# Performance work log

Measured on AMD Instinct MI355X. Metric: run time of the kernel, lower is better.

The kernel has to match this reference:

```python
import jax, jax.numpy as jnp
import numpy as np

NUM_SPECIES = 7
B, A, F = 1024, 48, 384


def setup_inputs() -> dict:
    key = jax.random.key(0)
    ks = jax.random.split(key, 10)
    species = jax.random.randint(ks[0], (B, A), 0, NUM_SPECIES, dtype=jnp.int32)
    aev = jax.random.normal(ks[1], (B, A, F), dtype=jnp.float32)
    def w(k, shape, fan_in):
        s = 1.0 / np.sqrt(fan_in).astype(np.float32)
        return jax.random.uniform(k, shape, jnp.float32, -s, s)
    return {
        "species": species,
        "aev": aev,
        "W1": w(ks[2], (NUM_SPECIES, 256, 384), 384),
        "b1": w(ks[3], (NUM_SPECIES, 256), 384),
        "W2": w(ks[4], (NUM_SPECIES, 192, 256), 256),
        "b2": w(ks[5], (NUM_SPECIES, 192), 256),
        "W3": w(ks[6], (NUM_SPECIES, 160, 192), 192),
        "b3": w(ks[7], (NUM_SPECIES, 160), 192),
        "W4": w(ks[8], (NUM_SPECIES, 1, 160), 160),
        "b4": w(ks[9], (NUM_SPECIES, 1), 160),
    }


def reference(species, aev, W1, b1, W2, b2, W3, b3, W4, b4):
    # species: [B, A] int, aev: [B, A, 384]
    celu = lambda x: jax.nn.celu(x, alpha=0.1)

    def expert(s):
        # Per-species MLP 384->256->192->160->1 applied to all atoms; selected via mask.
        h = celu(jnp.einsum('baf,hf->bah', aev, W1[s]) + b1[s])
        h = celu(jnp.einsum('bah,gh->bag', h, W2[s]) + b2[s])
        h = celu(jnp.einsum('bag,eg->bae', h, W3[s]) + b3[s])
        return (jnp.einsum('bae,oe->bao', h, W4[s]) + b4[s])[..., 0]  # [B, A]

    atom_energy = jnp.zeros(species.shape, aev.dtype)
    for s in range(NUM_SPECIES):  # fixed small expert loop (hard routing)
        atom_energy = jnp.where(species == s, expert(s), atom_energy)
    # scatter-sum atomic energies into per-molecule energies
    return atom_energy.sum(axis=1)  # [B]
```

## Files before the change

kernel.cpp:

```cpp
#include <hip/hip_runtime.h>
#include <math.h>

#define NSPEC 7
#define NMOL 1024
#define APM 48
#define NATOMS (NMOL * APM)
#define FDIM 384

typedef unsigned short u16;
typedef unsigned int u32;
typedef __attribute__((ext_vector_type(8))) short short8;
typedef __attribute__((ext_vector_type(4))) float floatx4;

#define W1_ELEMS_PER_S (16 * 12 * 64 * 8)
#define W2_ELEMS_PER_S (12 * 8 * 64 * 8)
#define W3_ELEMS_PER_S (10 * 6 * 64 * 8)

#define BUCKET_BLOCKS (NATOMS / 256)
#define PACK1_BLOCKS (NSPEC * 16)
#define PACK2_BLOCKS (NSPEC * 12)
#define PACK3_BLOCKS (NSPEC * 10)
#define PREP_BLOCKS (BUCKET_BLOCKS + PACK1_BLOCKS + PACK2_BLOCKS + PACK3_BLOCKS)

#define WS_W1_OFF 32
#define WS_W2_OFF (WS_W1_OFF + 1376256)
#define WS_W3_OFF (WS_W2_OFF + 688128)
#define WS_BKT_OFF (WS_W3_OFF + 430080)

#define BUFST 264

__device__ __forceinline__ float celu01(float x) {
    float e = fmaf(0.1f, __expf(x * 10.0f), -0.1f);
    return x > 0.0f ? x : e;
}

__device__ __forceinline__ u16 bfr(float f) {
    u32 u = __float_as_uint(f);
    u += 0x7fffu + ((u >> 16) & 1u);
    return (u16)(u >> 16);
}

__device__ __forceinline__ float bf2f(short s) {
    return __uint_as_float(((u32)(u16)s) << 16);
}

union U8 { short8 v; u16 u[8]; };

template <int KGS, int NTILES>
__device__ __forceinline__ void pack_tile(const float* __restrict__ W,
                                          u16* __restrict__ dst,
                                          int s, int t2, u16* lds) {
    const int K = KGS * 32;
    const int K4 = K / 4;
    int t = threadIdx.x;
    const float* wbase = W + ((size_t)(s * NTILES + t2) * 16) * K;
    for (int i = t; i < 16 * K4; i += 256) {
        int r = i / K4, c = i % K4;
        float4 v = ((const float4*)(wbase + (size_t)r * K))[c];
        u16* d = lds + r * K + c * 4;
        d[0] = bfr(v.x); d[1] = bfr(v.y); d[2] = bfr(v.z); d[3] = bfr(v.w);
    }
    __syncthreads();
    int w = t >> 6, lane = t & 63;
    int n = lane & 15, ks = lane >> 4;
    for (int kg = w; kg < KGS; kg += 4) {
        short8 v = *reinterpret_cast<const short8*>(lds + n * K + kg * 32 + ks * 8);
        *reinterpret_cast<short8*>(
            dst + (((size_t)(s * NTILES + t2) * KGS + kg) * 64 + lane) * 8) = v;
    }
}

__global__ void prep_kernel(const int* __restrict__ species,
                            int* __restrict__ g_cnt, u16* __restrict__ bucket,
                            const float* __restrict__ W1, const float* __restrict__ W2,
                            const float* __restrict__ W3,
                            u16* __restrict__ w1p, u16* __restrict__ w2p,
                            u16* __restrict__ w3p, float* __restrict__ out) {
    __shared__ u16 lds[16 * 384];
    __shared__ int l_cnt[NSPEC];
    __shared__ int l_base[NSPEC];
    int t = threadIdx.x;
    int bx = blockIdx.x;
    if (bx < BUCKET_BLOCKS) {
        if (bx == 0) {
            float4 z = {0.f, 0.f, 0.f, 0.f};
            ((float4*)out)[t] = z;
        }
        if (t < NSPEC) l_cnt[t] = 0;
        __syncthreads();
        int i = bx * 256 + t;
        int s = species[i];
        int lpos = atomicAdd(&l_cnt[s], 1);
        __syncthreads();
        if (t < NSPEC) l_base[t] = atomicAdd(&g_cnt[t], l_cnt[t]);
        __syncthreads();
        bucket[s * NATOMS + l_base[s] + lpos] = (u16)i;
    } else if (bx < BUCKET_BLOCKS + PACK1_BLOCKS) {
        int pid = bx - BUCKET_BLOCKS;
        pack_tile<12, 16>(W1, w1p, pid / 16, pid % 16, lds);
    } else if (bx < BUCKET_BLOCKS + PACK1_BLOCKS + PACK2_BLOCKS) {
        int pid = bx - (BUCKET_BLOCKS + PACK1_BLOCKS);
        pack_tile<8, 12>(W2, w2p, pid / 12, pid % 12, lds);
    } else {
        int pid = bx - (BUCKET_BLOCKS + PACK1_BLOCKS + PACK2_BLOCKS);
        pack_tile<6, 10>(W3, w3p, pid / 10, pid % 10, lds);
    }
}

template <int KGS, int NT, int NBUF>
__device__ __forceinline__ void run_layer(const short8* af0, const short8* af1,
                                          const u16* __restrict__ wsp,
                                          const float* __restrict__ bias,
                                          u16* __restrict__ outbuf, int lane) {
    const int nl = lane & 15, kg4 = lane >> 4;
    const u16* wb = wsp + (size_t)lane * 8;
    short8 b[NBUF][KGS];
#pragma unroll
    for (int p = 0; p < NBUF - 1; ++p)
#pragma unroll
        for (int kg = 0; kg < KGS; ++kg)
            b[p][kg] = *reinterpret_cast<const short8*>(wb + ((size_t)p * KGS + kg) * 512);
#pragma unroll
    for (int t = 0; t < NT; ++t) {
        int pre = t + NBUF - 1;
        if (pre < NT) {
            int slot = pre % NBUF;
#pragma unroll
            for (int kg = 0; kg < KGS; ++kg)
                b[slot][kg] = *reinterpret_cast<const short8*>(wb + ((size_t)pre * KGS + kg) * 512);
        }
        int cur = t % NBUF;
        floatx4 acc0 = {0.f, 0.f, 0.f, 0.f};
        floatx4 acc1 = {0.f, 0.f, 0.f, 0.f};
#pragma unroll
        for (int kg = 0; kg < KGS; ++kg) {
            acc0 = __builtin_amdgcn_mfma_f32_16x16x32_bf16(af0[kg], b[cur][kg], acc0, 0, 0, 0);
            acc1 = __builtin_amdgcn_mfma_f32_16x16x32_bf16(af1[kg], b[cur][kg], acc1, 0, 0, 0);
        }
        float bn = bias[t * 16 + nl];
#pragma unroll
        for (int r = 0; r < 4; ++r) {
            outbuf[(kg4 * 4 + r) * BUFST + t * 16 + nl] = bfr(celu01(acc0[r] + bn));
            outbuf[(16 + kg4 * 4 + r) * BUFST + t * 16 + nl] = bfr(celu01(acc1[r] + bn));
        }
    }
}

template <int KGS>
__device__ __forceinline__ void load_a_lds(const u16* __restrict__ buf,
                                           short8* af0, short8* af1, int lane) {
    int nl = lane & 15, kg4 = lane >> 4;
#pragma unroll
    for (int kg = 0; kg < KGS; ++kg) {
        af0[kg] = *reinterpret_cast<const short8*>(buf + (size_t)nl * BUFST + kg * 32 + kg4 * 8);
        af1[kg] = *reinterpret_cast<const short8*>(buf + (size_t)(16 + nl) * BUFST + kg * 32 + kg4 * 8);
    }
}

__global__ __launch_bounds__(128, 2) void mlp_kernel(
    const float* __restrict__ aev,
    const u16* __restrict__ w1p, const u16* __restrict__ w2p, const u16* __restrict__ w3p,
    const float* __restrict__ b1, const float* __restrict__ b2, const float* __restrict__ b3,
    const float* __restrict__ W4, const float* __restrict__ b4,
    const int* __restrict__ g_cnt, const u16* __restrict__ bucket,
    float* __restrict__ out) {
    int bx = blockIdx.x;
    int s = bx & 7;
    if (s >= NSPEC) return;
    int chunk = bx >> 3;
    int cnt = g_cnt[s];
    int w = threadIdx.x >> 6, lane = threadIdx.x & 63;
    int base = chunk * 64 + w * 32;
    if (base >= cnt) return;

    __shared__ __align__(16) u16 bufs[2][32 * BUFST];
    u16* buf = &bufs[w][0];

    int nl = lane & 15, kg4 = lane >> 4;

    short8 af0[12], af1[12];
    {
        int i0 = base + nl;       if (i0 >= cnt) i0 = cnt - 1;
        int i1 = base + 16 + nl;  if (i1 >= cnt) i1 = cnt - 1;
        int a0 = (int)bucket[s * NATOMS + i0];
        int a1 = (int)bucket[s * NATOMS + i1];
        const float* ar0 = aev + (size_t)a0 * FDIM;
        const float* ar1 = aev + (size_t)a1 * FDIM;
#pragma unroll
        for (int kg = 0; kg < 12; ++kg) {
            const float4* p0 = (const float4*)(ar0 + kg * 32 + kg4 * 8);
            const float4* p1 = (const float4*)(ar1 + kg * 32 + kg4 * 8);
            float4 a = p0[0], b = p0[1];
            float4 c = p1[0], d = p1[1];
            U8 x, y;
            x.u[0] = bfr(a.x); x.u[1] = bfr(a.y); x.u[2] = bfr(a.z); x.u[3] = bfr(a.w);
            x.u[4] = bfr(b.x); x.u[5] = bfr(b.y); x.u[6] = bfr(b.z); x.u[7] = bfr(b.w);
            y.u[0] = bfr(c.x); y.u[1] = bfr(c.y); y.u[2] = bfr(c.z); y.u[3] = bfr(c.w);
            y.u[4] = bfr(d.x); y.u[5] = bfr(d.y); y.u[6] = bfr(d.z); y.u[7] = bfr(d.w);
            af0[kg] = x.v;
            af1[kg] = y.v;
        }
    }
    run_layer<12, 16, 2>(af0, af1, w1p + (size_t)s * W1_ELEMS_PER_S, b1 + s * 256, buf, lane);

    short8 c0[8], c1[8];
    load_a_lds<8>(buf, c0, c1, lane);
    run_layer<8, 12, 3>(c0, c1, w2p + (size_t)s * W2_ELEMS_PER_S, b2 + s * 192, buf, lane);

    short8 d0[6], d1[6];
    load_a_lds<6>(buf, d0, d1, lane);
    run_layer<6, 10, 3>(d0, d1, w3p + (size_t)s * W3_ELEMS_PER_S, b3 + s * 160, buf, lane);

    {
        int m = lane >> 1, q = lane & 1;
        const u16* h = buf + (size_t)m * BUFST + q * 80;
        const float* w4s = W4 + s * 160 + q * 80;
        float p = 0.f;
#pragma unroll
        for (int c = 0; c < 10; ++c) {
            short8 hv = *reinterpret_cast<const short8*>(h + c * 8);
            const float4* wp4 = (const float4*)(w4s + c * 8);
            float4 wa = wp4[0], wb = wp4[1];
            p += bf2f(hv[0]) * wa.x + bf2f(hv[1]) * wa.y + bf2f(hv[2]) * wa.z + bf2f(hv[3]) * wa.w;
            p += bf2f(hv[4]) * wb.x + bf2f(hv[5]) * wb.y + bf2f(hv[6]) * wb.z + bf2f(hv[7]) * wb.w;
        }
        p += __shfl_down(p, 1, 2);
        int idx = base + m;
        if (q == 0 && idx < cnt) {
            int atom = (int)bucket[s * NATOMS + idx];
            atomicAdd(&out[atom / APM], p + b4[s]);
        }
    }
}

extern "C" void kernel_launch(void* const* d_in, const int* in_sizes, int n_in,
                              void* d_out, int out_size, void* d_ws, size_t ws_size,
                              hipStream_t stream) {
    const int* species = (const int*)d_in[0];
    const float* aev = (const float*)d_in[1];
    const float* W1 = (const float*)d_in[2];
    const float* b1 = (const float*)d_in[3];
    const float* W2 = (const float*)d_in[4];
    const float* b2 = (const float*)d_in[5];
    const float* W3 = (const float*)d_in[6];
    const float* b3 = (const float*)d_in[7];
    const float* W4 = (const float*)d_in[8];
    const float* b4 = (const float*)d_in[9];
    float* out = (float*)d_out;

    unsigned char* wsb = (unsigned char*)d_ws;
    int* g_cnt = (int*)wsb;
    u16* w1p = (u16*)(wsb + WS_W1_OFF);
    u16* w2p = (u16*)(wsb + WS_W2_OFF);
    u16* w3p = (u16*)(wsb + WS_W3_OFF);
    u16* bucket = (u16*)(wsb + WS_BKT_OFF);

    hipMemsetAsync(g_cnt, 0, 8 * sizeof(int), stream);

    prep_kernel<<<PREP_BLOCKS, 256, 0, stream>>>(
        species, g_cnt, bucket, W1, W2, W3, w1p, w2p, w3p, out);

    mlp_kernel<<<8 * (NATOMS / 64), 128, 0, stream>>>(
        aev, w1p, w2p, w3p, b1, b2, b3, W4, b4, g_cnt, bucket, out);
}
```

Before: 163.5 us.

## Fuse prep and MLP kernels into one cooperative persistent kernel with grid sync

Merges the bucketing/weight-packing kernel and the per-species MLP kernel into a single cooperative launch of 512 blocks of 128 threads, separated by a grid-wide sync. After the sync each block loops over up to 8 chunks of atoms for its species instead of launching one block per chunk. This removes a kernel launch and its inter-kernel gap, but it caps concurrency at 512 blocks, adds the cost of a grid barrier, and leaves fewer blocks doing the packing work.

```diff
diff --git a/kernel.cpp b/kernel.cpp
--- a/kernel.cpp
+++ b/kernel.cpp
@@ -1,5 +1,8 @@
 #include <hip/hip_runtime.h>
+#include <hip/hip_cooperative_groups.h>
 #include <math.h>
+
+namespace cg = cooperative_groups;
 
 #define NSPEC 7
 #define NMOL 1024
@@ -16,18 +19,15 @@
 #define W2_ELEMS_PER_S (12 * 8 * 64 * 8)
 #define W3_ELEMS_PER_S (10 * 6 * 64 * 8)
 
-#define BUCKET_BLOCKS (NATOMS / 256)
-#define PACK1_BLOCKS (NSPEC * 16)
-#define PACK2_BLOCKS (NSPEC * 12)
-#define PACK3_BLOCKS (NSPEC * 10)
-#define PREP_BLOCKS (BUCKET_BLOCKS + PACK1_BLOCKS + PACK2_BLOCKS + PACK3_BLOCKS)
-
 #define WS_W1_OFF 32
 #define WS_W2_OFF (WS_W1_OFF + 1376256)
 #define WS_W3_OFF (WS_W2_OFF + 688128)
 #define WS_BKT_OFF (WS_W3_OFF + 430080)
 
 #define BUFST 264
+#define GRID 512
+#define BUCKET_BLOCKS 384
+#define NTILE_TOTAL 266
 
 __device__ __forceinline__ float celu01(float x) {
     float e = fmaf(0.1f, __expf(x * 10.0f), -0.1f);
@@ -53,9 +53,9 @@
     const int K = KGS * 32;
     const int K4 = K / 4;
     int t = threadIdx.x;
-    const float* wbase = W + ((size_t)(s * NTILES + t2) * 16) * K;
-    for (int i = t; i < 16 * K4; i += 256) {
-        int r = i / K4, c = i % K4;
+    const float* wbase = W + (size_t)(s * NTILES + t2) * 16 * K;
+    for (int i = t; i < 16 * K4; i += 128) {
+        int r = i / K4, c = i - r * K4;
         float4 v = ((const float4*)(wbase + (size_t)r * K))[c];
         u16* d = lds + r * K + c * 4;
         d[0] = bfr(v.x); d[1] = bfr(v.y); d[2] = bfr(v.z); d[3] = bfr(v.w);
@@ -63,172 +63,173 @@
     __syncthreads();
     int w = t >> 6, lane = t & 63;
     int n = lane & 15, ks = lane >> 4;
-    for (int kg = w; kg < KGS; kg += 4) {
+    for (int kg = w; kg < KGS; kg += 2) {
         short8 v = *reinterpret_cast<const short8*>(lds + n * K + kg * 32 + ks * 8);
         *reinterpret_cast<short8*>(
             dst + (((size_t)(s * NTILES + t2) * KGS + kg) * 64 + lane) * 8) = v;
     }
-}
-
-__global__ void prep_kernel(const int* __restrict__ species,
-                            int* __restrict__ g_cnt, u16* __restrict__ bucket,
-                            const float* __restrict__ W1, const float* __restrict__ W2,
-                            const float* __restrict__ W3,
-                            u16* __restrict__ w1p, u16* __restrict__ w2p,
-                            u16* __restrict__ w3p, float* __restrict__ out) {
-    __shared__ u16 lds[16 * 384];
+    __syncthreads();
+}
+
+template <int KGS, int NT, int NBUF>
+__device__ __forceinline__ void run_layer(const short8* af0, const short8* af1,
+                                          const u16* wsp, const float* bias,
+                                          u16* outbuf, int lane) {
+    const int nl = lane & 15, kg4 = lane >> 4;
+    const u16* wb = wsp + (size_t)lane * 8;
+    short8 b[NBUF][KGS];
+#pragma unroll
+    for (int p = 0; p < NBUF - 1; ++p)
+#pragma unroll
+        for (int kg = 0; kg < KGS; ++kg)
+            b[p][kg] = *reinterpret_cast<const short8*>(wb + ((size_t)p * KGS + kg) * 512);
+#pragma unroll
+    for (int t = 0; t < NT; ++t) {
+        int pre = t + NBUF - 1;
+        if (pre < NT) {
+            int slot = pre % NBUF;
+#pragma unroll
+            for (int kg = 0; kg < KGS; ++kg)
+                b[slot][kg] = *reinterpret_cast<const short8*>(wb + ((size_t)pre * KGS + kg) * 512);
+        }
+        int cur = t % NBUF;
+        floatx4 acc0 = {0.f, 0.f, 0.f, 0.f};
+        floatx4 acc1 = {0.f, 0.f, 0.f, 0.f};
+#pragma unroll
+        for (int kg = 0; kg < KGS; ++kg) {
+            acc0 = __builtin_amdgcn_mfma_f32_16x16x32_bf16(af0[kg], b[cur][kg], acc0, 0, 0, 0);
+            acc1 = __builtin_amdgcn_mfma_f32_16x16x32_bf16(af1[kg], b[cur][kg], acc1, 0, 0, 0);
+        }
+        float bn = bias[t * 16 + nl];
+#pragma unroll
+        for (int r = 0; r < 4; ++r) {
+            outbuf[(kg4 * 4 + r) * BUFST + t * 16 + nl] = bfr(celu01(acc0[r] + bn));
+            outbuf[(16 + kg4 * 4 + r) * BUFST + t * 16 + nl] = bfr(celu01(acc1[r] + bn));
+        }
+    }
+}
+
+template <int KGS>
+__device__ __forceinline__ void load_a_lds(const u16* buf, short8* af0, short8* af1, int lane) {
+    int nl = lane & 15, kg4 = lane >> 4;
+#pragma unroll
+    for (int kg = 0; kg < KGS; ++kg) {
+        af0[kg] = *reinterpret_cast<const short8*>(buf + (size_t)nl * BUFST + kg * 32 + kg4 * 8);
+        af1[kg] = *reinterpret_cast<const short8*>(buf + (size_t)(16 + nl) * BUFST + kg * 32 + kg4 * 8);
+    }
+}
+
+__global__ __launch_bounds__(128, 2) void fused_kernel(
+    const int* species, const float* aev,
+    const float* W1, const float* W2, const float* W3,
+    const float* b1, const float* b2, const float* b3,
+    const float* W4, const float* b4,
+    int* g_cnt, u16* bucket,
+    u16* w1p, u16* w2p, u16* w3p,
+    float* out) {
+    __shared__ __align__(16) u16 smem[2 * 32 * BUFST];
     __shared__ int l_cnt[NSPEC];
     __shared__ int l_base[NSPEC];
+
+    int bx = blockIdx.x;
     int t = threadIdx.x;
-    int bx = blockIdx.x;
+
     if (bx < BUCKET_BLOCKS) {
         if (bx == 0) {
             float4 z = {0.f, 0.f, 0.f, 0.f};
             ((float4*)out)[t] = z;
+            ((float4*)out)[t + 128] = z;
         }
         if (t < NSPEC) l_cnt[t] = 0;
         __syncthreads();
-        int i = bx * 256 + t;
+        int i = bx * 128 + t;
         int s = species[i];
         int lpos = atomicAdd(&l_cnt[s], 1);
         __syncthreads();
         if (t < NSPEC) l_base[t] = atomicAdd(&g_cnt[t], l_cnt[t]);
         __syncthreads();
         bucket[s * NATOMS + l_base[s] + lpos] = (u16)i;
-    } else if (bx < BUCKET_BLOCKS + PACK1_BLOCKS) {
-        int pid = bx - BUCKET_BLOCKS;
-        pack_tile<12, 16>(W1, w1p, pid / 16, pid % 16, lds);
-    } else if (bx < BUCKET_BLOCKS + PACK1_BLOCKS + PACK2_BLOCKS) {
-        int pid = bx - (BUCKET_BLOCKS + PACK1_BLOCKS);
-        pack_tile<8, 12>(W2, w2p, pid / 12, pid % 12, lds);
     } else {
-        int pid = bx - (BUCKET_BLOCKS + PACK1_BLOCKS + PACK2_BLOCKS);
-        pack_tile<6, 10>(W3, w3p, pid / 10, pid % 10, lds);
-    }
-}
-
-template <int KGS, int NT, int NBUF>
-__device__ __forceinline__ void run_layer(const short8* af0, const short8* af1,
-                                          const u16* __restrict__ wsp,
-                                          const float* __restrict__ bias,
-                                          u16* __restrict__ outbuf, int lane) {
-    const int nl = lane & 15, kg4 = lane >> 4;
-    const u16* wb = wsp + (size_t)lane * 8;
-    short8 b[NBUF][KGS];
-#pragma unroll
-    for (int p = 0; p < NBUF - 1; ++p)
-#pragma unroll
-        for (int kg = 0; kg < KGS; ++kg)
-            b[p][kg] = *reinterpret_cast<const short8*>(wb + ((size_t)p * KGS + kg) * 512);
-#pragma unroll
-    for (int t = 0; t < NT; ++t) {
-        int pre = t + NBUF - 1;
-        if (pre < NT) {
-            int slot = pre % NBUF;
-#pragma unroll
-            for (int kg = 0; kg < KGS; ++kg)
-                b[slot][kg] = *reinterpret_cast<const short8*>(wb + ((size_t)pre * KGS + kg) * 512);
-        }
-        int cur = t % NBUF;
-        floatx4 acc0 = {0.f, 0.f, 0.f, 0.f};
-        floatx4 acc1 = {0.f, 0.f, 0.f, 0.f};
-#pragma unroll
-        for (int kg = 0; kg < KGS; ++kg) {
-            acc0 = __builtin_amdgcn_mfma_f32_16x16x32_bf16(af0[kg], b[cur][kg], acc0, 0, 0, 0);
-            acc1 = __builtin_amdgcn_mfma_f32_16x16x32_bf16(af1[kg], b[cur][kg], acc1, 0, 0, 0);
-        }
-        float bn = bias[t * 16 + nl];
-#pragma unroll
-        for (int r = 0; r < 4; ++r) {
-            outbuf[(kg4 * 4 + r) * BUFST + t * 16 + nl] = bfr(celu01(acc0[r] + bn));
-            outbuf[(16 + kg4 * 4 + r) * BUFST + t * 16 + nl] = bfr(celu01(acc1[r] + bn));
-        }
-    }
-}
-
-template <int KGS>
-__device__ __forceinline__ void load_a_lds(const u16* __restrict__ buf,
-                                           short8* af0, short8* af1, int lane) {
-    int nl = lane & 15, kg4 = lane >> 4;
-#pragma unroll
-    for (int kg = 0; kg < KGS; ++kg) {
-        af0[kg] = *reinterpret_cast<const short8*>(buf + (size_t)nl * BUFST + kg * 32 + kg4 * 8);
-        af1[kg] = *reinterpret_cast<const short8*>(buf + (size_t)(16 + nl) * BUFST + kg * 32 + kg4 * 8);
-    }
-}
-
-__global__ __launch_bounds__(128, 2) void mlp_kernel(
-    const float* __restrict__ aev,
-    const u16* __restrict__ w1p, const u16* __restrict__ w2p, const u16* __restrict__ w3p,
-    const float* __restrict__ b1, const float* __restrict__ b2, const float* __restrict__ b3,
-    const float* __restrict__ W4, const float* __restrict__ b4,
-    const int* __restrict__ g_cnt, const u16* __restrict__ bucket,
-    float* __restrict__ out) {
-    int bx = blockIdx.x;
+        for (int tile = bx - BUCKET_BLOCKS; tile < NTILE_TOTAL; tile += GRID - BUCKET_BLOCKS) {
+            if (tile < 112) {
+                pack_tile<12, 16>(W1, w1p, tile / 16, tile % 16, smem);
+            } else if (tile < 196) {
+                int u = tile - 112;
+                pack_tile<8, 12>(W2, w2p, u / 12, u % 12, smem);
+            } else {
+                int u = tile - 196;
+                pack_tile<6, 10>(W3, w3p, u / 10, u % 10, smem);
+            }
+        }
+    }
+
+    __threadfence();
+    cg::this_grid().sync();
+
     int s = bx & 7;
     if (s >= NSPEC) return;
-    int chunk = bx >> 3;
     int cnt = g_cnt[s];
-    int w = threadIdx.x >> 6, lane = threadIdx.x & 63;
-    int base = chunk * 64 + w * 32;
-    if (base >= cnt) return;
-
-    __shared__ __align__(16) u16 bufs[2][32 * BUFST];
-    u16* buf = &bufs[w][0];
-
+    int w = t >> 6, lane = t & 63;
     int nl = lane & 15, kg4 = lane >> 4;
-
-    short8 af0[12], af1[12];
-    {
-        int i0 = base + nl;       if (i0 >= cnt) i0 = cnt - 1;
-        int i1 = base + 16 + nl;  if (i1 >= cnt) i1 = cnt - 1;
-        int a0 = (int)bucket[s * NATOMS + i0];
-        int a1 = (int)bucket[s * NATOMS + i1];
-        const float* ar0 = aev + (size_t)a0 * FDIM;
-        const float* ar1 = aev + (size_t)a1 * FDIM;
-#pragma unroll
-        for (int kg = 0; kg < 12; ++kg) {
-            const float4* p0 = (const float4*)(ar0 + kg * 32 + kg4 * 8);
-            const float4* p1 = (const float4*)(ar1 + kg * 32 + kg4 * 8);
-            float4 a = p0[0], b = p0[1];
-            float4 c = p1[0], d = p1[1];
-            U8 x, y;
-            x.u[0] = bfr(a.x); x.u[1] = bfr(a.y); x.u[2] = bfr(a.z); x.u[3] = bfr(a.w);
-            x.u[4] = bfr(b.x); x.u[5] = bfr(b.y); x.u[6] = bfr(b.z); x.u[7] = bfr(b.w);
-            y.u[0] = bfr(c.x); y.u[1] = bfr(c.y); y.u[2] = bfr(c.z); y.u[3] = bfr(c.w);
-            y.u[4] = bfr(d.x); y.u[5] = bfr(d.y); y.u[6] = bfr(d.z); y.u[7] = bfr(d.w);
-            af0[kg] = x.v;
-            af1[kg] = y.v;
-        }
-    }
-    run_layer<12, 16, 2>(af0, af1, w1p + (size_t)s * W1_ELEMS_PER_S, b1 + s * 256, buf, lane);
-
-    short8 c0[8], c1[8];
-    load_a_lds<8>(buf, c0, c1, lane);
-    run_layer<8, 12, 3>(c0, c1, w2p + (size_t)s * W2_ELEMS_PER_S, b2 + s * 192, buf, lane);
-
-    short8 d0[6], d1[6];
-    load_a_lds<6>(buf, d0, d1, lane);
-    run_layer<6, 10, 3>(d0, d1, w3p + (size_t)s * W3_ELEMS_PER_S, b3 + s * 160, buf, lane);
-
-    {
-        int m = lane >> 1, q = lane & 1;
-        const u16* h = buf + (size_t)m * BUFST + q * 80;
-        const float* w4s = W4 + s * 160 + q * 80;
-        float p = 0.f;
-#pragma unroll
-        for (int c = 0; c < 10; ++c) {
-            short8 hv = *reinterpret_cast<const short8*>(h + c * 8);
-            const float4* wp4 = (const float4*)(w4s + c * 8);
-            float4 wa = wp4[0], wb = wp4[1];
-            p += bf2f(hv[0]) * wa.x + bf2f(hv[1]) * wa.y + bf2f(hv[2]) * wa.z + bf2f(hv[3]) * wa.w;
-            p += bf2f(hv[4]) * wb.x + bf2f(hv[5]) * wb.y + bf2f(hv[6]) * wb.z + bf2f(hv[7]) * wb.w;
-        }
-        p += __shfl_down(p, 1, 2);
-        int idx = base + m;
-        if (q == 0 && idx < cnt) {
-            int atom = (int)bucket[s * NATOMS + idx];
-            atomicAdd(&out[atom / APM], p + b4[s]);
+    u16* buf = smem + (size_t)w * (32 * BUFST);
+
+    for (int j = 0; j < 8; ++j) {
+        int chunk = (bx >> 3) + j * 64;
+        int base = chunk * 64 + w * 32;
+        if (base >= cnt) continue;
+
+        short8 af0[12], af1[12];
+        {
+            int i0 = base + nl;       if (i0 >= cnt) i0 = cnt - 1;
+            int i1 = base + 16 + nl;  if (i1 >= cnt) i1 = cnt - 1;
+            int a0 = (int)bucket[s * NATOMS + i0];
+            int a1 = (int)bucket[s * NATOMS + i1];
+            const float* ar0 = aev + (size_t)a0 * FDIM;
+            const float* ar1 = aev + (size_t)a1 * FDIM;
+#pragma unroll
+            for (int kg = 0; kg < 12; ++kg) {
+                const float4* p0 = (const float4*)(ar0 + kg * 32 + kg4 * 8);
+                const float4* p1 = (const float4*)(ar1 + kg * 32 + kg4 * 8);
+                float4 a = p0[0], b = p0[1];
+                float4 c = p1[0], d = p1[1];
+                U8 x, y;
+                x.u[0] = bfr(a.x); x.u[1] = bfr(a.y); x.u[2] = bfr(a.z); x.u[3] = bfr(a.w);
+                x.u[4] = bfr(b.x); x.u[5] = bfr(b.y); x.u[6] = bfr(b.z); x.u[7] = bfr(b.w);
+                y.u[0] = bfr(c.x); y.u[1] = bfr(c.y); y.u[2] = bfr(c.z); y.u[3] = bfr(c.w);
+                y.u[4] = bfr(d.x); y.u[5] = bfr(d.y); y.u[6] = bfr(d.z); y.u[7] = bfr(d.w);
+                af0[kg] = x.v;
+                af1[kg] = y.v;
+            }
+        }
+        run_layer<12, 16, 2>(af0, af1, w1p + (size_t)s * W1_ELEMS_PER_S, b1 + s * 256, buf, lane);
+
+        short8 c0[8], c1[8];
+        load_a_lds<8>(buf, c0, c1, lane);
+        run_layer<8, 12, 3>(c0, c1, w2p + (size_t)s * W2_ELEMS_PER_S, b2 + s * 192, buf, lane);
+
+        short8 d0[6], d1[6];
+        load_a_lds<6>(buf, d0, d1, lane);
+        run_layer<6, 10, 3>(d0, d1, w3p + (size_t)s * W3_ELEMS_PER_S, b3 + s * 160, buf, lane);
+
+        {
+            int m = lane >> 1, q = lane & 1;
+            const u16* h = buf + (size_t)m * BUFST + q * 80;
+            const float* w4s = W4 + s * 160 + q * 80;
+            float p = 0.f;
+#pragma unroll
+            for (int c = 0; c < 10; ++c) {
+                short8 hv = *reinterpret_cast<const short8*>(h + c * 8);
+                const float4* wp4 = (const float4*)(w4s + c * 8);
+                float4 wa = wp4[0], wb = wp4[1];
+                p += bf2f(hv[0]) * wa.x + bf2f(hv[1]) * wa.y + bf2f(hv[2]) * wa.z + bf2f(hv[3]) * wa.w;
+                p += bf2f(hv[4]) * wb.x + bf2f(hv[5]) * wb.y + bf2f(hv[6]) * wb.z + bf2f(hv[7]) * wb.w;
+            }
+            p += __shfl_down(p, 1, 2);
+            int idx = base + m;
+            if (q == 0 && idx < cnt) {
+                int atom = (int)bucket[s * NATOMS + idx];
+                atomicAdd(&out[atom / APM], p + b4[s]);
+            }
         }
     }
 }
@@ -257,9 +258,15 @@
 
     hipMemsetAsync(g_cnt, 0, 8 * sizeof(int), stream);
 
-    prep_kernel<<<PREP_BLOCKS, 256, 0, stream>>>(
-        species, g_cnt, bucket, W1, W2, W3, w1p, w2p, w3p, out);
-
-    mlp_kernel<<<8 * (NATOMS / 64), 128, 0, stream>>>(
-        aev, w1p, w2p, w3p, b1, b2, b3, W4, b4, g_cnt, bucket, out);
-}
+    void* args[] = {
+        (void*)&species, (void*)&aev,
+        (void*)&W1, (void*)&W2, (void*)&W3,
+        (void*)&b1, (void*)&b2, (void*)&b3,
+        (void*)&W4, (void*)&b4,
+        (void*)&g_cnt, (void*)&bucket,
+        (void*)&w1p, (void*)&w2p, (void*)&w3p,
+        (void*)&out,
+    };
+    hipLaunchCooperativeKernel((void*)fused_kernel, dim3(GRID), dim3(128),
+                               args, 0, stream);
+}
```

Result: slower. 609.4 us (+272.8%).

## Stage weight tiles through LDS with async global_load_lds double buffering

Applied to the files above, without the earlier changes.

The MLP kernel's weight tiles are now loaded cooperatively by both waves into a double-buffered LDS staging area via global_load_lds, instead of each wave loading its own copy from global into registers with a multi-deep register prefetch. This halves global/L2 weight traffic per block and frees registers, at the cost of a block-wide barrier per output tile. The prep kernel is also reshaped to 1024-thread blocks, with fewer bucketing blocks handling four atoms per thread. Both waves now run all layers even if the second wave's atoms exceed the count, since barriers require the whole block.

```diff
diff --git a/kernel.cpp b/kernel.cpp
--- a/kernel.cpp
+++ b/kernel.cpp
@@ -16,11 +16,9 @@
 #define W2_ELEMS_PER_S (12 * 8 * 64 * 8)
 #define W3_ELEMS_PER_S (10 * 6 * 64 * 8)
 
-#define BUCKET_BLOCKS (NATOMS / 256)
-#define PACK1_BLOCKS (NSPEC * 16)
-#define PACK2_BLOCKS (NSPEC * 12)
-#define PACK3_BLOCKS (NSPEC * 10)
-#define PREP_BLOCKS (BUCKET_BLOCKS + PACK1_BLOCKS + PACK2_BLOCKS + PACK3_BLOCKS)
+#define BKT_BLOCKS 12
+#define PACK_TILES 266
+#define PREP_BLOCKS (BKT_BLOCKS + PACK_TILES)
 
 #define WS_W1_OFF 32
 #define WS_W2_OFF (WS_W1_OFF + 1376256)
@@ -28,6 +26,7 @@
 #define WS_BKT_OFF (WS_W3_OFF + 430080)
 
 #define BUFST 264
+#define BSTW 6144
 
 __device__ __forceinline__ float celu01(float x) {
     float e = fmaf(0.1f, __expf(x * 10.0f), -0.1f);
@@ -53,89 +52,107 @@
     const int K = KGS * 32;
     const int K4 = K / 4;
     int t = threadIdx.x;
-    const float* wbase = W + ((size_t)(s * NTILES + t2) * 16) * K;
-    for (int i = t; i < 16 * K4; i += 256) {
-        int r = i / K4, c = i % K4;
+    const float* wbase = W + (size_t)(s * NTILES + t2) * 16 * K;
+    for (int i = t; i < 16 * K4; i += 1024) {
+        int r = i / K4, c = i - r * K4;
         float4 v = ((const float4*)(wbase + (size_t)r * K))[c];
         u16* d = lds + r * K + c * 4;
         d[0] = bfr(v.x); d[1] = bfr(v.y); d[2] = bfr(v.z); d[3] = bfr(v.w);
     }
     __syncthreads();
-    int w = t >> 6, lane = t & 63;
+    int wv = t >> 6, lane = t & 63;
     int n = lane & 15, ks = lane >> 4;
-    for (int kg = w; kg < KGS; kg += 4) {
+    for (int kg = wv; kg < KGS; kg += 16) {
         short8 v = *reinterpret_cast<const short8*>(lds + n * K + kg * 32 + ks * 8);
         *reinterpret_cast<short8*>(
             dst + (((size_t)(s * NTILES + t2) * KGS + kg) * 64 + lane) * 8) = v;
     }
 }
 
-__global__ void prep_kernel(const int* __restrict__ species,
-                            int* __restrict__ g_cnt, u16* __restrict__ bucket,
-                            const float* __restrict__ W1, const float* __restrict__ W2,
-                            const float* __restrict__ W3,
-                            u16* __restrict__ w1p, u16* __restrict__ w2p,
-                            u16* __restrict__ w3p, float* __restrict__ out) {
-    __shared__ u16 lds[16 * 384];
+__global__ __launch_bounds__(1024) void prep_kernel(
+    const int* __restrict__ species,
+    int* __restrict__ g_cnt, u16* __restrict__ bucket,
+    const float* __restrict__ W1, const float* __restrict__ W2,
+    const float* __restrict__ W3,
+    u16* __restrict__ w1p, u16* __restrict__ w2p, u16* __restrict__ w3p,
+    float* __restrict__ out) {
+    __shared__ __align__(16) u16 lds[16 * 384];
     __shared__ int l_cnt[NSPEC];
     __shared__ int l_base[NSPEC];
     int t = threadIdx.x;
     int bx = blockIdx.x;
-    if (bx < BUCKET_BLOCKS) {
-        if (bx == 0) {
-            float4 z = {0.f, 0.f, 0.f, 0.f};
-            ((float4*)out)[t] = z;
-        }
+    if (bx < BKT_BLOCKS) {
+        if (bx == 0) out[t] = 0.0f;
         if (t < NSPEC) l_cnt[t] = 0;
         __syncthreads();
-        int i = bx * 256 + t;
-        int s = species[i];
-        int lpos = atomicAdd(&l_cnt[s], 1);
+        int sp[4], lp[4];
+#pragma unroll
+        for (int j = 0; j < 4; ++j) {
+            int i = bx * 4096 + j * 1024 + t;
+            sp[j] = species[i];
+            lp[j] = atomicAdd(&l_cnt[sp[j]], 1);
+        }
         __syncthreads();
         if (t < NSPEC) l_base[t] = atomicAdd(&g_cnt[t], l_cnt[t]);
         __syncthreads();
-        bucket[s * NATOMS + l_base[s] + lpos] = (u16)i;
-    } else if (bx < BUCKET_BLOCKS + PACK1_BLOCKS) {
-        int pid = bx - BUCKET_BLOCKS;
-        pack_tile<12, 16>(W1, w1p, pid / 16, pid % 16, lds);
-    } else if (bx < BUCKET_BLOCKS + PACK1_BLOCKS + PACK2_BLOCKS) {
-        int pid = bx - (BUCKET_BLOCKS + PACK1_BLOCKS);
-        pack_tile<8, 12>(W2, w2p, pid / 12, pid % 12, lds);
+#pragma unroll
+        for (int j = 0; j < 4; ++j) {
+            int i = bx * 4096 + j * 1024 + t;
+            bucket[sp[j] * NATOMS + l_base[sp[j]] + lp[j]] = (u16)i;
+        }
     } else {
-        int pid = bx - (BUCKET_BLOCKS + PACK1_BLOCKS + PACK2_BLOCKS);
-        pack_tile<6, 10>(W3, w3p, pid / 10, pid % 10, lds);
-    }
-}
-
-template <int KGS, int NT, int NBUF>
+        int tile = bx - BKT_BLOCKS;
+        if (tile < 112) {
+            pack_tile<12, 16>(W1, w1p, tile / 16, tile % 16, lds);
+        } else if (tile < 196) {
+            int u = tile - 112;
+            pack_tile<8, 12>(W2, w2p, u / 12, u % 12, lds);
+        } else {
+            int u = tile - 196;
+            pack_tile<6, 10>(W3, w3p, u / 10, u % 10, lds);
+        }
+    }
+}
+
+template <int KGS>
+__device__ __forceinline__ void stage(const u16* __restrict__ gsrc,
+                                      u16* __restrict__ ldst, int tid) {
+    int w = tid >> 6, lane = tid & 63;
+#pragma unroll
+    for (int r = 0; r < KGS / 2; ++r) {
+        int off = r * 1024 + w * 512;
+        __builtin_amdgcn_global_load_lds(
+            (const __attribute__((address_space(1))) unsigned int*)(gsrc + off + lane * 8),
+            (__attribute__((address_space(3))) unsigned int*)(ldst + off),
+            16, 0, 0);
+    }
+}
+
+template <int KGS, int NT>
 __device__ __forceinline__ void run_layer(const short8* af0, const short8* af1,
                                           const u16* __restrict__ wsp,
                                           const float* __restrict__ bias,
-                                          u16* __restrict__ outbuf, int lane) {
+                                          u16* __restrict__ outbuf,
+                                          u16* __restrict__ bst,
+                                          int tid, int lane) {
     const int nl = lane & 15, kg4 = lane >> 4;
-    const u16* wb = wsp + (size_t)lane * 8;
-    short8 b[NBUF][KGS];
-#pragma unroll
-    for (int p = 0; p < NBUF - 1; ++p)
+    stage<KGS>(wsp, bst, tid);
+#pragma unroll
+    for (int t = 0; t < NT; ++t) {
+        __syncthreads();
+        if (t + 1 < NT)
+            stage<KGS>(wsp + (size_t)(t + 1) * (KGS * 512), bst + ((t + 1) & 1) * BSTW, tid);
+        const u16* bb = bst + (t & 1) * BSTW + lane * 8;
+        short8 bf[KGS];
 #pragma unroll
         for (int kg = 0; kg < KGS; ++kg)
-            b[p][kg] = *reinterpret_cast<const short8*>(wb + ((size_t)p * KGS + kg) * 512);
-#pragma unroll
-    for (int t = 0; t < NT; ++t) {
-        int pre = t + NBUF - 1;
-        if (pre < NT) {
-            int slot = pre % NBUF;
-#pragma unroll
-            for (int kg = 0; kg < KGS; ++kg)
-                b[slot][kg] = *reinterpret_cast<const short8*>(wb + ((size_t)pre * KGS + kg) * 512);
-        }
-        int cur = t % NBUF;
+            bf[kg] = *reinterpret_cast<const short8*>(bb + kg * 512);
         floatx4 acc0 = {0.f, 0.f, 0.f, 0.f};
         floatx4 acc1 = {0.f, 0.f, 0.f, 0.f};
 #pragma unroll
         for (int kg = 0; kg < KGS; ++kg) {
-            acc0 = __builtin_amdgcn_mfma_f32_16x16x32_bf16(af0[kg], b[cur][kg], acc0, 0, 0, 0);
-            acc1 = __builtin_amdgcn_mfma_f32_16x16x32_bf16(af1[kg], b[cur][kg], acc1, 0, 0, 0);
+            acc0 = __builtin_amdgcn_mfma_f32_16x16x32_bf16(af0[kg], bf[kg], acc0, 0, 0, 0);
+            acc1 = __builtin_amdgcn_mfma_f32_16x16x32_bf16(af1[kg], bf[kg], acc1, 0, 0, 0);
         }
         float bn = bias[t * 16 + nl];
 #pragma unroll
@@ -169,14 +186,16 @@
     if (s >= NSPEC) return;
     int chunk = bx >> 3;
     int cnt = g_cnt[s];
-    int w = threadIdx.x >> 6, lane = threadIdx.x & 63;
+    if (chunk * 64 >= cnt) return;
+
+    __shared__ __align__(16) u16 act[2][32 * BUFST];
+    __shared__ __align__(16) u16 bst[2][BSTW];
+
+    int tid = threadIdx.x;
+    int w = tid >> 6, lane = tid & 63;
+    int nl = lane & 15, kg4 = lane >> 4;
     int base = chunk * 64 + w * 32;
-    if (base >= cnt) return;
-
-    __shared__ __align__(16) u16 bufs[2][32 * BUFST];
-    u16* buf = &bufs[w][0];
-
-    int nl = lane & 15, kg4 = lane >> 4;
+    u16* buf = &act[w][0];
 
     short8 af0[12], af1[12];
     {
@@ -201,15 +220,19 @@
             af1[kg] = y.v;
         }
     }
-    run_layer<12, 16, 2>(af0, af1, w1p + (size_t)s * W1_ELEMS_PER_S, b1 + s * 256, buf, lane);
+
+    run_layer<12, 16>(af0, af1, w1p + (size_t)s * W1_ELEMS_PER_S, b1 + s * 256,
+                      buf, &bst[0][0], tid, lane);
 
     short8 c0[8], c1[8];
     load_a_lds<8>(buf, c0, c1, lane);
-    run_layer<8, 12, 3>(c0, c1, w2p + (size_t)s * W2_ELEMS_PER_S, b2 + s * 192, buf, lane);
+    run_layer<8, 12>(c0, c1, w2p + (size_t)s * W2_ELEMS_PER_S, b2 + s * 192,
+                     buf, &bst[0][0], tid, lane);
 
     short8 d0[6], d1[6];
     load_a_lds<6>(buf, d0, d1, lane);
-    run_layer<6, 10, 3>(d0, d1, w3p + (size_t)s * W3_ELEMS_PER_S, b3 + s * 160, buf, lane);
+    run_layer<6, 10>(d0, d1, w3p + (size_t)s * W3_ELEMS_PER_S, b3 + s * 160,
+                     buf, &bst[0][0], tid, lane);
 
     {
         int m = lane >> 1, q = lane & 1;
@@ -257,7 +280,7 @@
 
     hipMemsetAsync(g_cnt, 0, 8 * sizeof(int), stream);
 
-    prep_kernel<<<PREP_BLOCKS, 256, 0, stream>>>(
+    prep_kernel<<<PREP_BLOCKS, 1024, 0, stream>>>(
         species, g_cnt, bucket, W1, W2, W3, w1p, w2p, w3p, out);
 
     mlp_kernel<<<8 * (NATOMS / 64), 128, 0, stream>>>(
```

New measurement: 209.0 us. +27.8%, slower.

## Drop weight prepacking; load fp32 weights directly and convert in-kernel

Applied to the files above, without the earlier changes.

Removes the pre-pass that converted W1-W3 to bf16 in an MFMA-fragment layout, so the prep kernel now only buckets atoms. The MLP kernel reads fp32 weight rows straight from the original tensors and rounds them to bf16 in registers. A two-slot ping-pong prefetch replaces the configurable NBUF buffering. Pre-pass work goes away, but each block now reads twice the weight bytes with strided row accesses and repeats the conversion for every chunk, which raises L2 traffic.

```diff
diff --git a/kernel.cpp b/kernel.cpp
--- a/kernel.cpp
+++ b/kernel.cpp
@@ -12,20 +12,9 @@
 typedef __attribute__((ext_vector_type(8))) short short8;
 typedef __attribute__((ext_vector_type(4))) float floatx4;
 
-#define W1_ELEMS_PER_S (16 * 12 * 64 * 8)
-#define W2_ELEMS_PER_S (12 * 8 * 64 * 8)
-#define W3_ELEMS_PER_S (10 * 6 * 64 * 8)
-
 #define BUCKET_BLOCKS (NATOMS / 256)
-#define PACK1_BLOCKS (NSPEC * 16)
-#define PACK2_BLOCKS (NSPEC * 12)
-#define PACK3_BLOCKS (NSPEC * 10)
-#define PREP_BLOCKS (BUCKET_BLOCKS + PACK1_BLOCKS + PACK2_BLOCKS + PACK3_BLOCKS)
-
-#define WS_W1_OFF 32
-#define WS_W2_OFF (WS_W1_OFF + 1376256)
-#define WS_W3_OFF (WS_W2_OFF + 688128)
-#define WS_BKT_OFF (WS_W3_OFF + 430080)
+
+#define WS_BKT_OFF 32
 
 #define BUFST 264
 
@@ -46,102 +35,92 @@
 
 union U8 { short8 v; u16 u[8]; };
 
-template <int KGS, int NTILES>
-__device__ __forceinline__ void pack_tile(const float* __restrict__ W,
-                                          u16* __restrict__ dst,
-                                          int s, int t2, u16* lds) {
-    const int K = KGS * 32;
-    const int K4 = K / 4;
-    int t = threadIdx.x;
-    const float* wbase = W + ((size_t)(s * NTILES + t2) * 16) * K;
-    for (int i = t; i < 16 * K4; i += 256) {
-        int r = i / K4, c = i % K4;
-        float4 v = ((const float4*)(wbase + (size_t)r * K))[c];
-        u16* d = lds + r * K + c * 4;
-        d[0] = bfr(v.x); d[1] = bfr(v.y); d[2] = bfr(v.z); d[3] = bfr(v.w);
-    }
-    __syncthreads();
-    int w = t >> 6, lane = t & 63;
-    int n = lane & 15, ks = lane >> 4;
-    for (int kg = w; kg < KGS; kg += 4) {
-        short8 v = *reinterpret_cast<const short8*>(lds + n * K + kg * 32 + ks * 8);
-        *reinterpret_cast<short8*>(
-            dst + (((size_t)(s * NTILES + t2) * KGS + kg) * 64 + lane) * 8) = v;
-    }
+__device__ __forceinline__ short8 ld_frag(const float* __restrict__ p) {
+    float4 a = ((const float4*)p)[0];
+    float4 b = ((const float4*)p)[1];
+    U8 x;
+    x.u[0] = bfr(a.x); x.u[1] = bfr(a.y); x.u[2] = bfr(a.z); x.u[3] = bfr(a.w);
+    x.u[4] = bfr(b.x); x.u[5] = bfr(b.y); x.u[6] = bfr(b.z); x.u[7] = bfr(b.w);
+    return x.v;
 }
 
 __global__ void prep_kernel(const int* __restrict__ species,
                             int* __restrict__ g_cnt, u16* __restrict__ bucket,
-                            const float* __restrict__ W1, const float* __restrict__ W2,
-                            const float* __restrict__ W3,
-                            u16* __restrict__ w1p, u16* __restrict__ w2p,
-                            u16* __restrict__ w3p, float* __restrict__ out) {
-    __shared__ u16 lds[16 * 384];
+                            float* __restrict__ out) {
+    int t = threadIdx.x;
+    int bx = blockIdx.x;
+    if (bx == 0) {
+        float4 z = {0.f, 0.f, 0.f, 0.f};
+        ((float4*)out)[t] = z;
+    }
     __shared__ int l_cnt[NSPEC];
     __shared__ int l_base[NSPEC];
-    int t = threadIdx.x;
-    int bx = blockIdx.x;
-    if (bx < BUCKET_BLOCKS) {
-        if (bx == 0) {
-            float4 z = {0.f, 0.f, 0.f, 0.f};
-            ((float4*)out)[t] = z;
-        }
-        if (t < NSPEC) l_cnt[t] = 0;
-        __syncthreads();
-        int i = bx * 256 + t;
-        int s = species[i];
-        int lpos = atomicAdd(&l_cnt[s], 1);
-        __syncthreads();
-        if (t < NSPEC) l_base[t] = atomicAdd(&g_cnt[t], l_cnt[t]);
-        __syncthreads();
-        bucket[s * NATOMS + l_base[s] + lpos] = (u16)i;
-    } else if (bx < BUCKET_BLOCKS + PACK1_BLOCKS) {
-        int pid = bx - BUCKET_BLOCKS;
-        pack_tile<12, 16>(W1, w1p, pid / 16, pid % 16, lds);
-    } else if (bx < BUCKET_BLOCKS + PACK1_BLOCKS + PACK2_BLOCKS) {
-        int pid = bx - (BUCKET_BLOCKS + PACK1_BLOCKS);
-        pack_tile<8, 12>(W2, w2p, pid / 12, pid % 12, lds);
-    } else {
-        int pid = bx - (BUCKET_BLOCKS + PACK1_BLOCKS + PACK2_BLOCKS);
-        pack_tile<6, 10>(W3, w3p, pid / 10, pid % 10, lds);
-    }
-}
-
-template <int KGS, int NT, int NBUF>
+    if (t < NSPEC) l_cnt[t] = 0;
+    __syncthreads();
+    int i = bx * 256 + t;
+    int s = species[i];
+    int lpos = atomicAdd(&l_cnt[s], 1);
+    __syncthreads();
+    if (t < NSPEC) l_base[t] = atomicAdd(&g_cnt[t], l_cnt[t]);
+    __syncthreads();
+    bucket[s * NATOMS + l_base[s] + lpos] = (u16)i;
+}
+
+template <int KGS, int NT>
 __device__ __forceinline__ void run_layer(const short8* af0, const short8* af1,
-                                          const u16* __restrict__ wsp,
+                                          const float* __restrict__ wsp,
                                           const float* __restrict__ bias,
                                           u16* __restrict__ outbuf, int lane) {
     const int nl = lane & 15, kg4 = lane >> 4;
-    const u16* wb = wsp + (size_t)lane * 8;
-    short8 b[NBUF][KGS];
-#pragma unroll
-    for (int p = 0; p < NBUF - 1; ++p)
-#pragma unroll
-        for (int kg = 0; kg < KGS; ++kg)
-            b[p][kg] = *reinterpret_cast<const short8*>(wb + ((size_t)p * KGS + kg) * 512);
-#pragma unroll
-    for (int t = 0; t < NT; ++t) {
-        int pre = t + NBUF - 1;
-        if (pre < NT) {
-            int slot = pre % NBUF;
-#pragma unroll
-            for (int kg = 0; kg < KGS; ++kg)
-                b[slot][kg] = *reinterpret_cast<const short8*>(wb + ((size_t)pre * KGS + kg) * 512);
-        }
-        int cur = t % NBUF;
-        floatx4 acc0 = {0.f, 0.f, 0.f, 0.f};
-        floatx4 acc1 = {0.f, 0.f, 0.f, 0.f};
-#pragma unroll
-        for (int kg = 0; kg < KGS; ++kg) {
-            acc0 = __builtin_amdgcn_mfma_f32_16x16x32_bf16(af0[kg], b[cur][kg], acc0, 0, 0, 0);
-            acc1 = __builtin_amdgcn_mfma_f32_16x16x32_bf16(af1[kg], b[cur][kg], acc1, 0, 0, 0);
-        }
-        float bn = bias[t * 16 + nl];
-#pragma unroll
-        for (int r = 0; r < 4; ++r) {
-            outbuf[(kg4 * 4 + r) * BUFST + t * 16 + nl] = bfr(celu01(acc0[r] + bn));
-            outbuf[(16 + kg4 * 4 + r) * BUFST + t * 16 + nl] = bfr(celu01(acc1[r] + bn));
+    const int K = KGS * 32;
+    short8 bA[KGS], bB[KGS];
+    {
+        const float* wr = wsp + (size_t)nl * K + kg4 * 8;
+#pragma unroll
+        for (int kg = 0; kg < KGS; ++kg) bA[kg] = ld_frag(wr + kg * 32);
+    }
+#pragma unroll
+    for (int tt = 0; tt < NT / 2; ++tt) {
+        int t0 = 2 * tt;
+        {
+            const float* wr = wsp + (size_t)((t0 + 1) * 16 + nl) * K + kg4 * 8;
+#pragma unroll
+            for (int kg = 0; kg < KGS; ++kg) bB[kg] = ld_frag(wr + kg * 32);
+        }
+        {
+            floatx4 acc0 = {0.f, 0.f, 0.f, 0.f};
+            floatx4 acc1 = {0.f, 0.f, 0.f, 0.f};
+#pragma unroll
+            for (int kg = 0; kg < KGS; ++kg) {
+                acc0 = __builtin_amdgcn_mfma_f32_16x16x32_bf16(af0[kg], bA[kg], acc0, 0, 0, 0);
+                acc1 = __builtin_amdgcn_mfma_f32_16x16x32_bf16(af1[kg], bA[kg], acc1, 0, 0, 0);
+            }
+            float bn = bias[t0 * 16 + nl];
+#pragma unroll
+            for (int r = 0; r < 4; ++r) {
+                outbuf[(kg4 * 4 + r) * BUFST + t0 * 16 + nl] = bfr(celu01(acc0[r] + bn));
+                outbuf[(16 + kg4 * 4 + r) * BUFST + t0 * 16 + nl] = bfr(celu01(acc1[r] + bn));
+            }
+        }
+        if (t0 + 2 < NT) {
+            const float* wr = wsp + (size_t)((t0 + 2) * 16 + nl) * K + kg4 * 8;
+#pragma unroll
+            for (int kg = 0; kg < KGS; ++kg) bA[kg] = ld_frag(wr + kg * 32);
+        }
+        {
+            floatx4 acc0 = {0.f, 0.f, 0.f, 0.f};
+            floatx4 acc1 = {0.f, 0.f, 0.f, 0.f};
+#pragma unroll
+            for (int kg = 0; kg < KGS; ++kg) {
+                acc0 = __builtin_amdgcn_mfma_f32_16x16x32_bf16(af0[kg], bB[kg], acc0, 0, 0, 0);
+                acc1 = __builtin_amdgcn_mfma_f32_16x16x32_bf16(af1[kg], bB[kg], acc1, 0, 0, 0);
+            }
+            float bn = bias[(t0 + 1) * 16 + nl];
+#pragma unroll
+            for (int r = 0; r < 4; ++r) {
+                outbuf[(kg4 * 4 + r) * BUFST + (t0 + 1) * 16 + nl] = bfr(celu01(acc0[r] + bn));
+                outbuf[(16 + kg4 * 4 + r) * BUFST + (t0 + 1) * 16 + nl] = bfr(celu01(acc1[r] + bn));
+            }
         }
     }
 }
@@ -159,7 +138,7 @@
 
 __global__ __launch_bounds__(128, 2) void mlp_kernel(
     const float* __restrict__ aev,
-    const u16* __restrict__ w1p, const u16* __restrict__ w2p, const u16* __restrict__ w3p,
+    const float* __restrict__ W1, const float* __restrict__ W2, const float* __restrict__ W3,
     const float* __restrict__ b1, const float* __restrict__ b2, const float* __restrict__ b3,
     const float* __restrict__ W4, const float* __restrict__ b4,
     const int* __restrict__ g_cnt, const u16* __restrict__ bucket,
@@ -188,28 +167,20 @@
         const float* ar1 = aev + (size_t)a1 * FDIM;
 #pragma unroll
         for (int kg = 0; kg < 12; ++kg) {
-            const float4* p0 = (const float4*)(ar0 + kg * 32 + kg4 * 8);
-            const float4* p1 = (const float4*)(ar1 + kg * 32 + kg4 * 8);
-            float4 a = p0[0], b = p0[1];
-            float4 c = p1[0], d = p1[1];
-            U8 x, y;
-            x.u[0] = bfr(a.x); x.u[1] = bfr(a.y); x.u[2] = bfr(a.z); x.u[3] = bfr(a.w);
-            x.u[4] = bfr(b.x); x.u[5] = bfr(b.y); x.u[6] = bfr(b.z); x.u[7] = bfr(b.w);
-            y.u[0] = bfr(c.x); y.u[1] = bfr(c.y); y.u[2] = bfr(c.z); y.u[3] = bfr(c.w);
-            y.u[4] = bfr(d.x); y.u[5] = bfr(d.y); y.u[6] = bfr(d.z); y.u[7] = bfr(d.w);
-            af0[kg] = x.v;
-            af1[kg] = y.v;
-        }
-    }
-    run_layer<12, 16, 2>(af0, af1, w1p + (size_t)s * W1_ELEMS_PER_S, b1 + s * 256, buf, lane);
+            af0[kg] = ld_frag(ar0 + kg * 32 + kg4 * 8);
+            af1[kg] = ld_frag(ar1 + kg * 32 + kg4 * 8);
+        }
+    }
+
+    run_layer<12, 16>(af0, af1, W1 + (size_t)s * 256 * 384, b1 + s * 256, buf, lane);
 
     short8 c0[8], c1[8];
     load_a_lds<8>(buf, c0, c1, lane);
-    run_layer<8, 12, 3>(c0, c1, w2p + (size_t)s * W2_ELEMS_PER_S, b2 + s * 192, buf, lane);
+    run_layer<8, 12>(c0, c1, W2 + (size_t)s * 192 * 256, b2 + s * 192, buf, lane);
 
     short8 d0[6], d1[6];
     load_a_lds<6>(buf, d0, d1, lane);
-    run_layer<6, 10, 3>(d0, d1, w3p + (size_t)s * W3_ELEMS_PER_S, b3 + s * 160, buf, lane);
+    run_layer<6, 10>(d0, d1, W3 + (size_t)s * 160 * 192, b3 + s * 160, buf, lane);
 
     {
         int m = lane >> 1, q = lane & 1;
@@ -250,16 +221,12 @@
 
     unsigned char* wsb = (unsigned char*)d_ws;
     int* g_cnt = (int*)wsb;
-    u16* w1p = (u16*)(wsb + WS_W1_OFF);
-    u16* w2p = (u16*)(wsb + WS_W2_OFF);
-    u16* w3p = (u16*)(wsb + WS_W3_OFF);
     u16* bucket = (u16*)(wsb + WS_BKT_OFF);
 
     hipMemsetAsync(g_cnt, 0, 8 * sizeof(int), stream);
 
-    prep_kernel<<<PREP_BLOCKS, 256, 0, stream>>>(
-        species, g_cnt, bucket, W1, W2, W3, w1p, w2p, w3p, out);
+    prep_kernel<<<BUCKET_BLOCKS, 256, 0, stream>>>(species, g_cnt, bucket, out);
 
     mlp_kernel<<<8 * (NATOMS / 64), 128, 0, stream>>>(
-        aev, w1p, w2p, w3p, b1, b2, b3, W4, b4, g_cnt, bucket, out);
-}
+        aev, W1, W2, W3, b1, b2, b3, W4, b4, g_cnt, bucket, out);
+}
```

Measured after the change: 428.2 us. +161.9%, slower.
